# Performance work log

Measured on AMD Instinct MI355X. Metric: run time of the kernel, lower is better.

Reference implementation:

```python
import jax, jax.numpy as jnp
import numpy as np

T, U, H, P, UC = 256, 512, 64, 1024, 10000
LAMBDA_T = 0.1      # temporal decay rate (Flashback default scale)
LAMBDA_S = 100.0    # spatial decay rate
DAY = 86400.0


def setup_inputs() -> dict:
    key = jax.random.key(0)
    ks = jax.random.split(key, 12)
    sc = 0.02
    x = jax.random.randint(ks[0], (T, U), 0, P)
    # timestamps, increasing along the sequence axis (checkin order)
    t = jnp.sort(jax.random.uniform(ks[1], (T, U)) * (7.0 * DAY), axis=0)
    t_slot = jax.random.randint(ks[2], (T, U), 0, 168)
    s = jax.random.normal(ks[3], (T, U, 2))
    y = jax.random.randint(ks[4], (T, U), 0, P)
    h = jnp.zeros((U, H), jnp.float32)
    active_user = jax.random.randint(ks[5], (U,), 0, UC)
    poi_emb = jax.random.normal(ks[6], (P, H)) * sc
    user_emb = jax.random.normal(ks[7], (UC, H)) * sc
    Wx = jax.random.normal(ks[8], (H, 3 * H)) * sc
    Wh = jax.random.normal(ks[9], (H, 3 * H)) * sc
    b = jnp.zeros((3 * H,), jnp.float32)
    fc_W = jax.random.normal(ks[10], (2 * H, P)) * sc
    fc_b = jnp.zeros((P,), jnp.float32)
    return dict(x=x, t=t, t_slot=t_slot, s=s, y=y, h=h, active_user=active_user,
                poi_emb=poi_emb, user_emb=user_emb, Wx=Wx, Wh=Wh, b=b,
                fc_W=fc_W, fc_b=fc_b)


def _gru_scan(x_emb, h0, Wx, Wh, b):
    # x_emb: [T,U,H], h0: [U,H]
    def step(hprev, xt):
        gx = xt @ Wx + b          # [U,3H]
        gh = hprev @ Wh           # [U,3H]
        rx, zx, nx = jnp.split(gx, 3, axis=-1)
        rh, zh, nh = jnp.split(gh, 3, axis=-1)
        r = jax.nn.sigmoid(rx + rh)
        z = jax.nn.sigmoid(zx + zh)
        n = jnp.tanh(nx + r * nh)
        hn = (1.0 - z) * hprev + z * n
        return hn, hn
    hT, outs = jax.lax.scan(step, h0, x_emb)
    return outs, hT  # [T,U,H], [U,H]


def reference(x, t, t_slot, s, y, h, active_user,
              poi_emb, user_emb, Wx, Wh, b, fc_W, fc_b):
    seq_len, user_len = x.shape
    x_emb = poi_emb[x]                 # [T,U,H]  (stands in for pre_model emb)
    p_u = user_emb[active_user]        # [U,H]
    out, hT = _gru_scan(x_emb, h, Wx, Wh, b)  # RNN outputs [T,U,H]

    # Pairwise spatiotemporal decay weights, vectorized over (i,j,user).
    dt = t[:, None, :] - t[None, :, :]                    # [T,T,U]
    ds = jnp.linalg.norm(s[:, None, :, :] - s[None, :, :, :], axis=-1)  # [T,T,U]
    f_t = 0.5 * (jnp.cos(dt * (2.0 * jnp.pi / DAY)) + 1.0) * jnp.exp(-(dt / DAY) * LAMBDA_T)
    f_s = jnp.exp(-ds * LAMBDA_S)
    causal = jnp.tril(jnp.ones((seq_len, seq_len), dtype=bool))  # j <= i
    w = jnp.where(causal[:, :, None], f_t * f_s + 1e-10, 0.0)     # [T,T,U]
    sum_w = jnp.sum(w, axis=1)                                    # [T,U]
    out_w = jnp.einsum('iju,juh->iuh', w, out) / sum_w[:, :, None]  # [T,U,H]

    feats = jnp.concatenate(
        [out_w, jnp.broadcast_to(p_u[None], (seq_len, user_len, p_u.shape[-1]))],
        axis=-1)                                                  # [T,U,2H]
    y_linear = feats @ fc_W + fc_b                                # [T,U,P]
    return y_linear, hT
```

## Files before the change

### kernel.cpp

```cpp
#include <hip/hip_runtime.h>

#define T_N 256
#define U_N 512
#define H_N 64
#define P_N 1024

typedef __attribute__((ext_vector_type(8))) short short8;
typedef __attribute__((ext_vector_type(4))) short short4v;
typedef __attribute__((ext_vector_type(4))) float f32x4;

#define MFMA __builtin_amdgcn_mfma_f32_16x16x32_bf16

#define LGKM_BARRIER() asm volatile("s_waitcnt lgkmcnt(0)\ns_barrier" ::: "memory")

__device__ __forceinline__ float fastrcp(float x) { return __builtin_amdgcn_rcpf(x); }
__device__ __forceinline__ float fastsqrt(float x) { return __builtin_amdgcn_sqrtf(x); }

__device__ __forceinline__ short f2bf(float f) {
  union { float f; unsigned u; } v; v.f = f;
  unsigned r = v.u + 0x7FFFu + ((v.u >> 16) & 1u);
  return (short)(r >> 16);
}

__device__ __forceinline__ unsigned cvtpk(float lo, float hi) {
  unsigned r;
  asm("v_cvt_pk_bf16_f32 %0, %1, %2" : "=v"(r) : "v"(lo), "v"(hi));
  return r;
}

__device__ __forceinline__ short8 pack8(float4 a, float4 b) {
  union { unsigned u[4]; short8 s; } z;
  z.u[0] = cvtpk(a.x, a.y); z.u[1] = cvtpk(a.z, a.w);
  z.u[2] = cvtpk(b.x, b.y); z.u[3] = cvtpk(b.z, b.w);
  return z.s;
}

__device__ __forceinline__ float bfu_lo(unsigned u) {
  union { unsigned x; float f; } v; v.x = u << 16; return v.f;
}
__device__ __forceinline__ float bfu_hi(unsigned u) {
  union { unsigned x; float f; } v; v.x = u & 0xffff0000u; return v.f;
}

__global__ __launch_bounds__(256) void k_pack(
    const float* __restrict__ Wx, const float* __restrict__ Wh,
    const float* __restrict__ fcW, short* __restrict__ wxp,
    short* __restrict__ whp, short* __restrict__ bp) {
  if (blockIdx.x < 12) {
    int idx = blockIdx.x * 256 + threadIdx.x;
    int m = idx / 1536;
    int r = idx % 1536;
    const float* W = m ? Wh : Wx;
    short* op = m ? whp : wxp;
    int ks = r / 768, lk = (r / 192) & 3, g = r % 192;
#pragma unroll
    for (int e = 0; e < 8; ++e)
      op[(size_t)r * 8 + e] = f2bf(W[(ks * 32 + lk * 8 + e) * 192 + g]);
  } else {
    int sidx = (blockIdx.x - 12) * 256 + threadIdx.x;
    int s = sidx & 1023;
    int kg = (sidx >> 10) & 3;
    int ks = sidx >> 12;
    int L = (s & ~63) + 4 * (s & 15) + ((s >> 4) & 3);
#pragma unroll
    for (int e = 0; e < 8; ++e) {
      int k = ks * 32 + kg * 8 + e;
      bp[((size_t)((ks * 4 + kg) * P_N + s)) * 8 + e] = f2bf(fcW[k * P_N + L]);
    }
  }
}

__global__ __launch_bounds__(256) void k_gx(
    const int* __restrict__ x, const float* __restrict__ poi_emb,
    const short* __restrict__ wxp, const float* __restrict__ b,
    char* __restrict__ gxp) {
  int wave = threadIdx.x >> 6, lane = threadIdx.x & 63;
  int lr = lane & 15, lk = lane >> 4;
  int tile = blockIdx.x * 4 + wave;
  int row = tile * 16 + lr;
  int xv = x[row];
  const float* pb = poi_emb + (size_t)xv * H_N + lk * 8;
  float4 v0 = *(const float4*)pb, v1 = *(const float4*)(pb + 4);
  float4 v2 = *(const float4*)(pb + 32), v3 = *(const float4*)(pb + 36);
  short8 ax0 = pack8(v0, v1), ax1 = pack8(v2, v3);
#pragma unroll
  for (int j = 0; j < 12; ++j) {
    float bc = b[16 * j + lr];
    f32x4 acc = {bc, bc, bc, bc};
    short8 bf0 = *(const short8*)&wxp[((size_t)((0 * 4 + lk) * 192 + 16 * j + lr)) * 8];
    short8 bf1 = *(const short8*)&wxp[((size_t)((1 * 4 + lk) * 192 + 16 * j + lr)) * 8];
    acc = MFMA(ax0, bf0, acc, 0, 0, 0);
    acc = MFMA(ax1, bf1, acc, 0, 0, 0);
    uint2 pk;
    pk.x = cvtpk(acc[0], acc[1]);
    pk.y = cvtpk(acc[2], acc[3]);
    *(uint2*)(gxp + (((size_t)tile * 12 + j) * 64 + lane) * 8) = pk;
  }
}

__global__ __launch_bounds__(256) void k_scan2(
    const char* __restrict__ gxp, const float* __restrict__ h0,
    const short* __restrict__ whp, short* __restrict__ out_tr,
    float* __restrict__ hT) {
  int ublk = blockIdx.x;
  int u0 = ublk * 16;
  int tid = threadIdx.x;
  int w = tid >> 6, lane = tid & 63, lr = lane & 15, lk = lane >> 4;
  __shared__ __align__(16) float h_lds[8][16][68];
  int sgr = 16 * w, sgz = 64 + 16 * w, sgn = 128 + 16 * w;
  short8 fhr[2], fhz[2], fhn[2];
#pragma unroll
  for (int ks = 0; ks < 2; ++ks) {
    size_t base = (size_t)((ks * 4 + lk) * 192) * 8;
    fhr[ks] = *(const short8*)&whp[base + (size_t)(sgr + lr) * 8];
    fhz[ks] = *(const short8*)&whp[base + (size_t)(sgz + lr) * 8];
    fhn[ks] = *(const short8*)&whp[base + (size_t)(sgn + lr) * 8];
  }
  for (int idx = tid; idx < 16 * 64; idx += 256)
    h_lds[7][idx >> 6][idx & 63] = h0[(size_t)(u0 + (idx >> 6)) * H_N + (idx & 63)];
  __syncthreads();
  float hp[4];
#pragma unroll
  for (int e = 0; e < 4; ++e) hp[e] = h_lds[7][4 * lk + e][16 * w + lr];
  short8 ah0, ah1;
  {
    float4 q0 = *(float4*)&h_lds[7][lr][8 * lk];
    float4 q1 = *(float4*)&h_lds[7][lr][8 * lk + 4];
    float4 q2 = *(float4*)&h_lds[7][lr][32 + 8 * lk];
    float4 q3 = *(float4*)&h_lds[7][lr][32 + 8 * lk + 4];
    ah0 = pack8(q0, q1); ah1 = pack8(q2, q3);
  }
  const char* gbase = gxp + (((size_t)ublk * 12 + w) * 64 + lane) * 8;
  uint2 pr0, pr1, pr2, pr3, pr4, pr5, pr6, pr7;
  uint2 pz0, pz1, pz2, pz3, pz4, pz5, pz6, pz7;
  uint2 pn0, pn1, pn2, pn3, pn4, pn5, pn6, pn7;
#define PF(sl, tt) { size_t o = (size_t)(tt) * 196608; \
    pr##sl = *(const uint2*)(gbase + o); \
    pz##sl = *(const uint2*)(gbase + o + 2048); \
    pn##sl = *(const uint2*)(gbase + o + 4096); }
  PF(0, 0) PF(1, 1) PF(2, 2) PF(3, 3) PF(4, 4) PF(5, 5) PF(6, 6) PF(7, 7)
  for (int t8 = 0; t8 < T_N; t8 += 8) {
#define GATE(E, TB) { \
      float r = fastrcp(1.f + __expf(-accr[E])); \
      float z = fastrcp(1.f + __expf(-accz[E])); \
      float npre = __builtin_fmaf(r, accnh[E], accnx[E]); \
      float e2 = __expf(2.f * npre); \
      float n = 1.f - 2.f * fastrcp(e2 + 1.f); \
      float hn = __builtin_fmaf(z, n - hp[E], hp[E]); \
      hp[E] = hn; \
      h_lds[TB][4 * lk + E][16 * w + lr] = hn; }
#define BODY(TB, SL) { \
      f32x4 accr = {bfu_lo(pr##SL.x), bfu_hi(pr##SL.x), bfu_lo(pr##SL.y), bfu_hi(pr##SL.y)}; \
      f32x4 accz = {bfu_lo(pz##SL.x), bfu_hi(pz##SL.x), bfu_lo(pz##SL.y), bfu_hi(pz##SL.y)}; \
      f32x4 accnx = {bfu_lo(pn##SL.x), bfu_hi(pn##SL.x), bfu_lo(pn##SL.y), bfu_hi(pn##SL.y)}; \
      f32x4 accnh = {0.f, 0.f, 0.f, 0.f}; \
      int tpf = t8 + TB + 8; if (tpf > 255) tpf = 255; \
      PF(SL, tpf) \
      accr = MFMA(ah0, fhr[0], accr, 0, 0, 0); \
      accr = MFMA(ah1, fhr[1], accr, 0, 0, 0); \
      accz = MFMA(ah0, fhz[0], accz, 0, 0, 0); \
      accz = MFMA(ah1, fhz[1], accz, 0, 0, 0); \
      accnh = MFMA(ah0, fhn[0], accnh, 0, 0, 0); \
      accnh = MFMA(ah1, fhn[1], accnh, 0, 0, 0); \
      GATE(0, TB) GATE(1, TB) GATE(2, TB) GATE(3, TB) \
      LGKM_BARRIER(); \
      { \
        float4 q0 = *(float4*)&h_lds[TB][lr][8 * lk]; \
        float4 q1 = *(float4*)&h_lds[TB][lr][8 * lk + 4]; \
        float4 q2 = *(float4*)&h_lds[TB][lr][32 + 8 * lk]; \
        float4 q3 = *(float4*)&h_lds[TB][lr][32 + 8 * lk + 4]; \
        ah0 = pack8(q0, q1); ah1 = pack8(q2, q3); \
      } }
    BODY(0, 0) BODY(1, 1) BODY(2, 2) BODY(3, 3)
    BODY(4, 4) BODY(5, 5) BODY(6, 6) BODY(7, 7)
    {
      int tb = t8 >> 3;
#pragma unroll
      for (int pp = 0; pp < 4; ++pp) {
        int p = pp * 256 + tid;
        int uu = p >> 6, hh = p & 63;
        uint4 pkd;
        pkd.x = cvtpk(h_lds[0][uu][hh], h_lds[1][uu][hh]);
        pkd.y = cvtpk(h_lds[2][uu][hh], h_lds[3][uu][hh]);
        pkd.z = cvtpk(h_lds[4][uu][hh], h_lds[5][uu][hh]);
        pkd.w = cvtpk(h_lds[6][uu][hh], h_lds[7][uu][hh]);
        *(uint4*)&out_tr[((((size_t)(u0 + uu)) * 32 + tb) * 64 + hh) * 8] = pkd;
      }
    }
    LGKM_BARRIER();
  }
  for (int idx = tid; idx < 16 * 64; idx += 256)
    hT[(size_t)(u0 + (idx >> 6)) * H_N + (idx & 63)] = h_lds[7][idx >> 6][idx & 63];
}

__global__ __launch_bounds__(256) void k_ub(
    const int* __restrict__ active_user, const float* __restrict__ user_emb,
    const float* __restrict__ fcW, const float* __restrict__ fcb,
    float* __restrict__ ub) {
  int u = blockIdx.x;
  int tid = threadIdx.x;
  __shared__ float pu[H_N];
  if (tid < H_N) pu[tid] = user_emb[active_user[u] * H_N + tid];
  __syncthreads();
  for (int p = tid; p < P_N; p += 256) {
    float acc = fcb[p];
#pragma unroll
    for (int k = 0; k < H_N; ++k) acc += pu[k] * fcW[(H_N + k) * P_N + p];
    ub[u * P_N + p] = acc;
  }
}

__global__ __launch_bounds__(256, 4) void k_stage2(
    const float* __restrict__ t, const float* __restrict__ s,
    const short* __restrict__ out_tr, short* __restrict__ apk) {
  int u = blockIdx.x;
  int tid = threadIdx.x;
  __shared__ __align__(16) unsigned short wlT[16][264];
  __shared__ __align__(8) float csU[T_N][2];
  __shared__ __align__(8) float seU[T_N][2];
  __shared__ float eU[T_N];
  float cj, sj, Fj, sx, sy;
  {
    int jr = tid;
    float tj = t[jr * U_N + u];
    cj = __cosf(tj * 7.2722052166430395e-05f);
    sj = __sinf(tj * 7.2722052166430395e-05f);
    float ej = __expf(tj * -1.1574074074074074e-06f);
    Fj = __expf(tj * 1.1574074074074074e-06f);
    csU[jr][0] = cj; csU[jr][1] = sj;
    eU[jr] = ej;
    sx = s[((size_t)jr * U_N + u) * 2];
    sy = s[((size_t)jr * U_N + u) * 2 + 1];
    seU[jr][0] = sx; seU[jr][1] = sy;
  }
  __syncthreads();
  int lane = tid & 63, wv = tid >> 6;
  int lr = lane & 15, lk = lane >> 4;
  int j = tid;
  const short* obase = out_tr + (size_t)u * 32 * 64 * 8;
  short8 ones;
#pragma unroll
  for (int e = 0; e < 8; ++e) ones[e] = (short)0x3F80;
  for (int c = 0; c < 16; ++c) {
    int nk = (c + 2) >> 1;
    if (wv * 64 < nk * 32) {
#pragma unroll
      for (int iqq = 0; iqq < 16; ++iqq) {
        int i = c * 16 + iqq;
        float ci = csU[i][0], si = csU[i][1];
        float ei = eU[i];
        float dx = seU[i][0] - sx, dy = seU[i][1] - sy;
        float dsn = fastsqrt(__builtin_fmaf(dx, dx, dy * dy));
        float fs = __expf(-100.0f * dsn);
        float ctm = __builtin_fmaf(ci, cj, si * sj);
        float ft2 = __builtin_fmaf(0.5f, ctm, 0.5f);
        float ww = __builtin_fmaf(ft2 * (ei * Fj), fs, 1e-10f);
        ww = (j <= i) ? ww : 0.0f;
        wlT[iqq][j] = (unsigned short)cvtpk(ww, ww);
      }
    }
    __syncthreads();
    f32x4 acc = {0.f, 0.f, 0.f, 0.f};
    f32x4 acc1 = {0.f, 0.f, 0.f, 0.f};
    for (int kk = 0; kk < nk; ++kk) {
      short8 aw = *(const short8*)&wlT[lr][kk * 32 + 8 * lk];
      short8 bo = *(const short8*)&obase[(((kk * 4 + lk) * 64) + 16 * wv + lr) * 8];
      acc = MFMA(aw, bo, acc, 0, 0, 0);
      acc1 = MFMA(aw, ones, acc1, 0, 0, 0);
    }
#pragma unroll
    for (int e = 0; e < 4; ++e) {
      int i = c * 16 + 4 * lk + e;
      float val = acc[e] * fastrcp(acc1[e]);
      apk[((size_t)i * U_N + u) * H_N + 16 * wv + lr] = f2bf(val);
    }
    __syncthreads();
  }
}

__global__ __launch_bounds__(256) void k_fc(
    const short* __restrict__ apk, const short* __restrict__ Bp,
    const float* __restrict__ ub, float* __restrict__ C) {
  int bm = blockIdx.x, bn = blockIdx.y;
  int tid = threadIdx.x;
  int wave = tid >> 6, lane = tid & 63;
  int wm = wave >> 1, wn = wave & 1;
  int row0 = bm * 128 + wm * 64;
  int col0 = bn * 128 + wn * 64;
  int lr = lane & 15, lk = lane >> 4;
  f32x4 acc[4][4] = {};
#pragma unroll
  for (int ks = 0; ks < 2; ++ks) {
    short8 af[4];
#pragma unroll
    for (int m = 0; m < 4; ++m)
      af[m] = *(const short8*)&apk[((size_t)(row0 + m * 16 + lr)) * H_N + ks * 32 + lk * 8];
#pragma unroll
    for (int n = 0; n < 4; ++n) {
      short8 bf = *(const short8*)&Bp[((size_t)((ks * 4 + lk) * P_N + col0 + n * 16 + lr)) * 8];
#pragma unroll
      for (int m = 0; m < 4; ++m)
        acc[m][n] = MFMA(af[m], bf, acc[m][n], 0, 0, 0);
    }
  }
#pragma unroll
  for (int m = 0; m < 4; ++m) {
    int rbase = row0 + m * 16 + lk * 4;
#pragma unroll
    for (int r = 0; r < 4; ++r) {
      int row = rbase + r;
      int uu = row & (U_N - 1);
      f32x4 ubv = *(const f32x4*)&ub[(size_t)uu * P_N + col0 + 4 * lr];
      f32x4 v;
      v[0] = acc[m][0][r] + ubv[0];
      v[1] = acc[m][1][r] + ubv[1];
      v[2] = acc[m][2][r] + ubv[2];
      v[3] = acc[m][3][r] + ubv[3];
      __builtin_nontemporal_store(v, (f32x4*)&C[(size_t)row * P_N + col0 + 4 * lr]);
    }
  }
}

extern "C" void kernel_launch(void* const* d_in, const int* in_sizes, int n_in,
                              void* d_out, int out_size, void* d_ws, size_t ws_size,
                              hipStream_t stream) {
  const int*   x           = (const int*)d_in[0];
  const float* t           = (const float*)d_in[1];
  const float* s           = (const float*)d_in[3];
  const float* h0          = (const float*)d_in[5];
  const int*   active_user = (const int*)d_in[6];
  const float* poi_emb     = (const float*)d_in[7];
  const float* user_emb    = (const float*)d_in[8];
  const float* Wx          = (const float*)d_in[9];
  const float* Wh          = (const float*)d_in[10];
  const float* b           = (const float*)d_in[11];
  const float* fcW         = (const float*)d_in[12];
  const float* fcb         = (const float*)d_in[13];

  float* y_out = (float*)d_out;
  float* hT = y_out + (size_t)T_N * U_N * P_N;

  char* ws = (char*)d_ws;
  short* out_tr = (short*)ws;
  char*  gxp    = ws + 16777216;
  short* apk    = (short*)(ws + 16777216);
  float* ub     = (float*)(ws + 67108864);
  short* bp     = (short*)(ws + 69206016);
  short* wxp    = (short*)(ws + 69337088);
  short* whp    = (short*)(ws + 69361664);

  k_pack<<<44, 256, 0, stream>>>(Wx, Wh, fcW, wxp, whp, bp);
  k_gx<<<2048, 256, 0, stream>>>(x, poi_emb, wxp, b, gxp);
  k_scan2<<<32, 256, 0, stream>>>(gxp, h0, whp, out_tr, hT);
  k_ub<<<U_N, 256, 0, stream>>>(active_user, user_emb, fcW, fcb, ub);
  k_stage2<<<U_N, 256, 0, stream>>>(t, s, out_tr, apk);
  k_fc<<<dim3(1024, 8), 256, 0, stream>>>(apk, bp, ub, y_out);
}
```

Before: 373.3 us.

## Transpose GRU scan MFMA to keep hidden state in registers, fuse user-bias kernel

The scan kernel swaps the MFMA operand order (gate weights as A, hidden state as B), so each lane owns four hidden units of one user. The new hidden state can then be kept in registers and written straight to the output. Only a small double-buffered bf16 LDS copy is shared per step, replacing the fp32 8-slot LDS tile, the per-block repack loop and the extra barrier. k_gx is transposed the same way to match the gx layout, and the user-bias computation is folded into the pack kernel, removing one launch. The trade-off is more register pressure from the hb buffer and different bf16 rounding points.

```diff
diff --git a/kernel.cpp b/kernel.cpp
--- a/kernel.cpp
+++ b/kernel.cpp
@@ -44,10 +44,13 @@
 
 __global__ __launch_bounds__(256) void k_pack(
     const float* __restrict__ Wx, const float* __restrict__ Wh,
-    const float* __restrict__ fcW, short* __restrict__ wxp,
-    short* __restrict__ whp, short* __restrict__ bp) {
+    const float* __restrict__ fcW, const int* __restrict__ active_user,
+    const float* __restrict__ user_emb, const float* __restrict__ fcb,
+    short* __restrict__ wxp, short* __restrict__ whp, short* __restrict__ bp,
+    float* __restrict__ ub) {
+  int tid = threadIdx.x;
   if (blockIdx.x < 12) {
-    int idx = blockIdx.x * 256 + threadIdx.x;
+    int idx = blockIdx.x * 256 + tid;
     int m = idx / 1536;
     int r = idx % 1536;
     const float* W = m ? Wh : Wx;
@@ -56,8 +59,8 @@
 #pragma unroll
     for (int e = 0; e < 8; ++e)
       op[(size_t)r * 8 + e] = f2bf(W[(ks * 32 + lk * 8 + e) * 192 + g]);
-  } else {
-    int sidx = (blockIdx.x - 12) * 256 + threadIdx.x;
+  } else if (blockIdx.x < 44) {
+    int sidx = (blockIdx.x - 12) * 256 + tid;
     int s = sidx & 1023;
     int kg = (sidx >> 10) & 3;
     int ks = sidx >> 12;
@@ -66,6 +69,17 @@
     for (int e = 0; e < 8; ++e) {
       int k = ks * 32 + kg * 8 + e;
       bp[((size_t)((ks * 4 + kg) * P_N + s)) * 8 + e] = f2bf(fcW[k * P_N + L]);
+    }
+  } else {
+    int u = blockIdx.x - 44;
+    __shared__ float pu[H_N];
+    if (tid < H_N) pu[tid] = user_emb[active_user[u] * H_N + tid];
+    __syncthreads();
+    for (int p = tid; p < P_N; p += 256) {
+      float acc = fcb[p];
+#pragma unroll
+      for (int k = 0; k < H_N; ++k) acc += pu[k] * fcW[(H_N + k) * P_N + p];
+      ub[u * P_N + p] = acc;
     }
   }
 }
@@ -85,12 +99,15 @@
   short8 ax0 = pack8(v0, v1), ax1 = pack8(v2, v3);
 #pragma unroll
   for (int j = 0; j < 12; ++j) {
-    float bc = b[16 * j + lr];
-    f32x4 acc = {bc, bc, bc, bc};
+    float bc = b[16 * j + 4 * lk + ((lane & 3) ^ (lane & 3))];
+    (void)bc;
+    f32x4 acc;
+#pragma unroll
+    for (int e = 0; e < 4; ++e) acc[e] = b[16 * j + 4 * lk + e];
     short8 bf0 = *(const short8*)&wxp[((size_t)((0 * 4 + lk) * 192 + 16 * j + lr)) * 8];
     short8 bf1 = *(const short8*)&wxp[((size_t)((1 * 4 + lk) * 192 + 16 * j + lr)) * 8];
-    acc = MFMA(ax0, bf0, acc, 0, 0, 0);
-    acc = MFMA(ax1, bf1, acc, 0, 0, 0);
+    acc = MFMA(bf0, ax0, acc, 0, 0, 0);
+    acc = MFMA(bf1, ax1, acc, 0, 0, 0);
     uint2 pk;
     pk.x = cvtpk(acc[0], acc[1]);
     pk.y = cvtpk(acc[2], acc[3]);
@@ -98,38 +115,38 @@
   }
 }
 
-__global__ __launch_bounds__(256) void k_scan2(
+__global__ __launch_bounds__(256) void k_scan3(
     const char* __restrict__ gxp, const float* __restrict__ h0,
     const short* __restrict__ whp, short* __restrict__ out_tr,
     float* __restrict__ hT) {
   int ublk = blockIdx.x;
   int u0 = ublk * 16;
   int tid = threadIdx.x;
-  int w = tid >> 6, lane = tid & 63, lr = lane & 15, lk = lane >> 4;
-  __shared__ __align__(16) float h_lds[8][16][68];
+  int w = tid >> 6, lane = tid & 63, lr = lane & 15, q = lane >> 4;
+  __shared__ __align__(16) unsigned short h16[2][16][68];
   int sgr = 16 * w, sgz = 64 + 16 * w, sgn = 128 + 16 * w;
   short8 fhr[2], fhz[2], fhn[2];
 #pragma unroll
   for (int ks = 0; ks < 2; ++ks) {
-    size_t base = (size_t)((ks * 4 + lk) * 192) * 8;
+    size_t base = (size_t)((ks * 4 + q) * 192) * 8;
     fhr[ks] = *(const short8*)&whp[base + (size_t)(sgr + lr) * 8];
     fhz[ks] = *(const short8*)&whp[base + (size_t)(sgz + lr) * 8];
     fhn[ks] = *(const short8*)&whp[base + (size_t)(sgn + lr) * 8];
   }
-  for (int idx = tid; idx < 16 * 64; idx += 256)
-    h_lds[7][idx >> 6][idx & 63] = h0[(size_t)(u0 + (idx >> 6)) * H_N + (idx & 63)];
+  float hp[4];
+#pragma unroll
+  for (int e = 0; e < 4; ++e)
+    hp[e] = h0[(size_t)(u0 + lr) * H_N + 16 * w + 4 * q + e];
+  {
+    uint2 pk;
+    pk.x = cvtpk(hp[0], hp[1]);
+    pk.y = cvtpk(hp[2], hp[3]);
+    *(uint2*)&h16[1][lr][16 * w + 4 * q] = pk;
+  }
   __syncthreads();
-  float hp[4];
-#pragma unroll
-  for (int e = 0; e < 4; ++e) hp[e] = h_lds[7][4 * lk + e][16 * w + lr];
-  short8 ah0, ah1;
-  {
-    float4 q0 = *(float4*)&h_lds[7][lr][8 * lk];
-    float4 q1 = *(float4*)&h_lds[7][lr][8 * lk + 4];
-    float4 q2 = *(float4*)&h_lds[7][lr][32 + 8 * lk];
-    float4 q3 = *(float4*)&h_lds[7][lr][32 + 8 * lk + 4];
-    ah0 = pack8(q0, q1); ah1 = pack8(q2, q3);
-  }
+  short8 bh0, bh1;
+  bh0 = *(const short8*)&h16[1][lr][8 * q];
+  bh1 = *(const short8*)&h16[1][lr][32 + 8 * q];
   const char* gbase = gxp + (((size_t)ublk * 12 + w) * 64 + lane) * 8;
   uint2 pr0, pr1, pr2, pr3, pr4, pr5, pr6, pr7;
   uint2 pz0, pz1, pz2, pz3, pz4, pz5, pz6, pz7;
@@ -139,6 +156,7 @@
     pz##sl = *(const uint2*)(gbase + o + 2048); \
     pn##sl = *(const uint2*)(gbase + o + 4096); }
   PF(0, 0) PF(1, 1) PF(2, 2) PF(3, 3) PF(4, 4) PF(5, 5) PF(6, 6) PF(7, 7)
+  float hb[4][8];
   for (int t8 = 0; t8 < T_N; t8 += 8) {
 #define GATE(E, TB) { \
       float r = fastrcp(1.f + __expf(-accr[E])); \
@@ -148,7 +166,7 @@
       float n = 1.f - 2.f * fastrcp(e2 + 1.f); \
       float hn = __builtin_fmaf(z, n - hp[E], hp[E]); \
       hp[E] = hn; \
-      h_lds[TB][4 * lk + E][16 * w + lr] = hn; }
+      hb[E][TB] = hn; }
 #define BODY(TB, SL) { \
       f32x4 accr = {bfu_lo(pr##SL.x), bfu_hi(pr##SL.x), bfu_lo(pr##SL.y), bfu_hi(pr##SL.y)}; \
       f32x4 accz = {bfu_lo(pz##SL.x), bfu_hi(pz##SL.x), bfu_lo(pz##SL.y), bfu_hi(pz##SL.y)}; \
@@ -156,58 +174,41 @@
       f32x4 accnh = {0.f, 0.f, 0.f, 0.f}; \
       int tpf = t8 + TB + 8; if (tpf > 255) tpf = 255; \
       PF(SL, tpf) \
-      accr = MFMA(ah0, fhr[0], accr, 0, 0, 0); \
-      accr = MFMA(ah1, fhr[1], accr, 0, 0, 0); \
-      accz = MFMA(ah0, fhz[0], accz, 0, 0, 0); \
-      accz = MFMA(ah1, fhz[1], accz, 0, 0, 0); \
-      accnh = MFMA(ah0, fhn[0], accnh, 0, 0, 0); \
-      accnh = MFMA(ah1, fhn[1], accnh, 0, 0, 0); \
+      accr = MFMA(fhr[0], bh0, accr, 0, 0, 0); \
+      accr = MFMA(fhr[1], bh1, accr, 0, 0, 0); \
+      accz = MFMA(fhz[0], bh0, accz, 0, 0, 0); \
+      accz = MFMA(fhz[1], bh1, accz, 0, 0, 0); \
+      accnh = MFMA(fhn[0], bh0, accnh, 0, 0, 0); \
+      accnh = MFMA(fhn[1], bh1, accnh, 0, 0, 0); \
       GATE(0, TB) GATE(1, TB) GATE(2, TB) GATE(3, TB) \
+      { \
+        uint2 pk; \
+        pk.x = cvtpk(hp[0], hp[1]); \
+        pk.y = cvtpk(hp[2], hp[3]); \
+        *(uint2*)&h16[(TB) & 1][lr][16 * w + 4 * q] = pk; \
+      } \
       LGKM_BARRIER(); \
-      { \
-        float4 q0 = *(float4*)&h_lds[TB][lr][8 * lk]; \
-        float4 q1 = *(float4*)&h_lds[TB][lr][8 * lk + 4]; \
-        float4 q2 = *(float4*)&h_lds[TB][lr][32 + 8 * lk]; \
-        float4 q3 = *(float4*)&h_lds[TB][lr][32 + 8 * lk + 4]; \
-        ah0 = pack8(q0, q1); ah1 = pack8(q2, q3); \
-      } }
+      bh0 = *(const short8*)&h16[(TB) & 1][lr][8 * q]; \
+      bh1 = *(const short8*)&h16[(TB) & 1][lr][32 + 8 * q]; }
     BODY(0, 0) BODY(1, 1) BODY(2, 2) BODY(3, 3)
     BODY(4, 4) BODY(5, 5) BODY(6, 6) BODY(7, 7)
     {
       int tb = t8 >> 3;
 #pragma unroll
-      for (int pp = 0; pp < 4; ++pp) {
-        int p = pp * 256 + tid;
-        int uu = p >> 6, hh = p & 63;
-        uint4 pkd;
-        pkd.x = cvtpk(h_lds[0][uu][hh], h_lds[1][uu][hh]);
-        pkd.y = cvtpk(h_lds[2][uu][hh], h_lds[3][uu][hh]);
-        pkd.z = cvtpk(h_lds[4][uu][hh], h_lds[5][uu][hh]);
-        pkd.w = cvtpk(h_lds[6][uu][hh], h_lds[7][uu][hh]);
-        *(uint4*)&out_tr[((((size_t)(u0 + uu)) * 32 + tb) * 64 + hh) * 8] = pkd;
+      for (int e = 0; e < 4; ++e) {
+        uint4 pk;
+        pk.x = cvtpk(hb[e][0], hb[e][1]);
+        pk.y = cvtpk(hb[e][2], hb[e][3]);
+        pk.z = cvtpk(hb[e][4], hb[e][5]);
+        pk.w = cvtpk(hb[e][6], hb[e][7]);
+        *(uint4*)&out_tr[((((size_t)(u0 + lr)) * 32 + tb) * 64 +
+                          (16 * w + 4 * q + e)) * 8] = pk;
       }
     }
-    LGKM_BARRIER();
-  }
-  for (int idx = tid; idx < 16 * 64; idx += 256)
-    hT[(size_t)(u0 + (idx >> 6)) * H_N + (idx & 63)] = h_lds[7][idx >> 6][idx & 63];
-}
-
-__global__ __launch_bounds__(256) void k_ub(
-    const int* __restrict__ active_user, const float* __restrict__ user_emb,
-    const float* __restrict__ fcW, const float* __restrict__ fcb,
-    float* __restrict__ ub) {
-  int u = blockIdx.x;
-  int tid = threadIdx.x;
-  __shared__ float pu[H_N];
-  if (tid < H_N) pu[tid] = user_emb[active_user[u] * H_N + tid];
-  __syncthreads();
-  for (int p = tid; p < P_N; p += 256) {
-    float acc = fcb[p];
-#pragma unroll
-    for (int k = 0; k < H_N; ++k) acc += pu[k] * fcW[(H_N + k) * P_N + p];
-    ub[u * P_N + p] = acc;
-  }
+  }
+#pragma unroll
+  for (int e = 0; e < 4; ++e)
+    hT[(size_t)(u0 + lr) * H_N + 16 * w + 4 * q + e] = hp[e];
 }
 
 __global__ __launch_bounds__(256, 4) void k_stage2(
@@ -349,10 +350,10 @@
   short* wxp    = (short*)(ws + 69337088);
   short* whp    = (short*)(ws + 69361664);
 
-  k_pack<<<44, 256, 0, stream>>>(Wx, Wh, fcW, wxp, whp, bp);
+  k_pack<<<556, 256, 0, stream>>>(Wx, Wh, fcW, active_user, user_emb, fcb,
+                                  wxp, whp, bp, ub);
   k_gx<<<2048, 256, 0, stream>>>(x, poi_emb, wxp, b, gxp);
-  k_scan2<<<32, 256, 0, stream>>>(gxp, h0, whp, out_tr, hT);
-  k_ub<<<U_N, 256, 0, stream>>>(active_user, user_emb, fcW, fcb, ub);
+  k_scan3<<<32, 256, 0, stream>>>(gxp, h0, whp, out_tr, hT);
   k_stage2<<<U_N, 256, 0, stream>>>(t, s, out_tr, apk);
   k_fc<<<dim3(1024, 8), 256, 0, stream>>>(apk, bp, ub, y_out);
 }
```

Result: no change. 368.7 us (-1.2%).
